# Performance work log

Hardware: AMD Instinct MI355X
Metric: run time of the kernel (lower is better)

## Reference

```python
import jax, jax.numpy as jnp
import numpy as np

F = 26          # categorical fields
VOCAB = 10000   # per-field vocab
ED = 64         # embed_dim
NUM = 13        # numerical_num
B = 4096        # batch
E = 8           # expert_num
T = 2           # task_num
D = (F + 1) * ED            # embed_output_dim = 1728
BOT = [512, 256]
TOW = [128, 64]


def setup_inputs() -> dict:
    key = jax.random.key(0)
    ks = jax.random.split(key, 20)
    s = 0.02
    inp = {}
    inp['categorical_x'] = jax.random.randint(ks[0], (B, F), 0, VOCAB, dtype=jnp.int64 if jax.config.read('jax_enable_x64') else jnp.int32)
    inp['numerical_x'] = jax.random.normal(ks[1], (B, NUM), dtype=jnp.float32)
    # shared embedding table with per-field offsets (pytorch-fm EmbeddingLayer)
    inp['offsets'] = jnp.arange(F, dtype=jnp.int32) * VOCAB
    inp['W_emb'] = jax.random.normal(ks[2], (F * VOCAB, ED), dtype=jnp.float32) * s
    # numerical linear
    inp['Wn'] = jax.random.normal(ks[3], (NUM, ED), dtype=jnp.float32) * s
    inp['bn'] = jnp.zeros((ED,), dtype=jnp.float32)
    # experts (stacked): D -> 512 -> 256, ReLU after each (BN/dropout identity at eval)
    inp['We1'] = jax.random.normal(ks[4], (E, D, BOT[0]), dtype=jnp.float32) * s
    inp['be1'] = jnp.zeros((E, BOT[0]), dtype=jnp.float32)
    inp['We2'] = jax.random.normal(ks[5], (E, BOT[0], BOT[1]), dtype=jnp.float32) * s
    inp['be2'] = jnp.zeros((E, BOT[1]), dtype=jnp.float32)
    # gates: D -> E with softmax
    inp['Wg'] = jax.random.normal(ks[6], (T, D, E), dtype=jnp.float32) * s
    inp['bg'] = jnp.zeros((T, E), dtype=jnp.float32)
    # towers: 256 -> 128 -> 64 -> 1
    inp['Wt1'] = jax.random.normal(ks[7], (T, BOT[1], TOW[0]), dtype=jnp.float32) * s
    inp['bt1'] = jnp.zeros((T, TOW[0]), dtype=jnp.float32)
    inp['Wt2'] = jax.random.normal(ks[8], (T, TOW[0], TOW[1]), dtype=jnp.float32) * s
    inp['bt2'] = jnp.zeros((T, TOW[1]), dtype=jnp.float32)
    inp['Wt3'] = jax.random.normal(ks[9], (T, TOW[1], 1), dtype=jnp.float32) * s
    inp['bt3'] = jnp.zeros((T, 1), dtype=jnp.float32)
    return inp


def reference(categorical_x, numerical_x, offsets, W_emb, Wn, bn,
              We1, be1, We2, be2, Wg, bg,
              Wt1, bt1, Wt2, bt2, Wt3, bt3):
    b = categorical_x.shape[0]
    cat_emb = W_emb[categorical_x + offsets[None, :]]          # [B, F, ED]
    num_emb = numerical_x @ Wn + bn                            # [B, ED]
    emb = jnp.concatenate([cat_emb, num_emb[:, None, :]], axis=1).reshape(b, -1)  # [B, D]
    # all experts on the shared embedding (duplicate() gives identical copies per task)
    h = jax.nn.relu(jnp.einsum('bd,edh->ebh', emb, We1) + be1[:, None, :])        # [E, B, 512]
    fea = jax.nn.relu(jnp.einsum('ebh,eho->ebo', h, We2) + be2[:, None, :])       # [E, B, 256]
    # per-task softmax gating and weighted expert mixing
    gate = jax.nn.softmax(jnp.einsum('bd,tde->tbe', emb, Wg) + bg[:, None, :], axis=-1)  # [T, B, E]
    task_fea = jnp.einsum('tbe,ebo->tbo', gate, fea)                              # [T, B, 256]
    # towers
    h1 = jax.nn.relu(jnp.einsum('tbo,toh->tbh', task_fea, Wt1) + bt1[:, None, :])
    h2 = jax.nn.relu(jnp.einsum('tbh,thk->tbk', h1, Wt2) + bt2[:, None, :])
    logits = jnp.einsum('tbk,tko->tbo', h2, Wt3) + bt3[:, None, :]                # [T, B, 1]
    return jax.nn.sigmoid(logits[..., 0])                                         # [T, B]
```

## Files before the change

kernel.cpp:

```cpp
#include <hip/hip_runtime.h>
#include <hip/hip_bf16.h>

#define B_SZ 4096
#define F_CAT 26
#define NUM_N 13
#define ED 64
#define D_DIM 1728
#define E_EXP 8
#define T_TASK 2
#define BOT0 512
#define BOT1 256
#define TOW0 128
#define TOW1 64

typedef __bf16 bf16x8 __attribute__((ext_vector_type(8)));
typedef float f32x4 __attribute__((ext_vector_type(4)));
typedef long lx2 __attribute__((ext_vector_type(2)));

__device__ __forceinline__ void gload_lds16(const void* g, void* l) {
  __builtin_amdgcn_global_load_lds(
      (const __attribute__((address_space(1))) void*)g,
      (__attribute__((address_space(3))) void*)l, 16, 0, 0);
}

#define BAR() do { asm volatile("" ::: "memory"); __builtin_amdgcn_s_barrier(); asm volatile("" ::: "memory"); } while (0)
#define VM6() asm volatile("s_waitcnt vmcnt(6)" ::: "memory")
#define VM4() asm volatile("s_waitcnt vmcnt(4)" ::: "memory")

__device__ __forceinline__ int permk(int k6) {
  return (k6 & 7) + (((k6 >> 3) & 3) << 4) + (((k6 >> 5) & 1) << 3);
}

__device__ __forceinline__ unsigned char f2e4m3(float x) {
  unsigned su = (__float_as_uint(x) >> 24) & 0x80u;
  float ax = fabsf(x);
  if (!(ax < 448.f)) return (unsigned char)(su | 0x7E);
  if (ax == 0.f) return (unsigned char)su;
  int e;
  float m = frexpf(ax, &e);
  int E = e - 1;
  if (E < -6) {
    int mi = (int)rintf(ldexpf(ax, 9));
    if (mi >= 8) return (unsigned char)(su | 0x08);
    return (unsigned char)(su | mi);
  }
  int mi = (int)rintf(ldexpf(m, 4));
  if (mi == 16) { mi = 8; E += 1; if (E > 8) return (unsigned char)(su | 0x7E); }
  return (unsigned char)(su | ((E + 7) << 3) | (mi - 8));
}

__device__ __forceinline__ void trans_tile_bf16(
    const float* __restrict__ inp, __hip_bfloat16* __restrict__ outp,
    int R, int C, int cx, int ry, float (*tile)[33])
{
  int c0 = cx * 32, r0 = ry * 32;
  int tx = threadIdx.x & 31, ty = threadIdx.x >> 5;
#pragma unroll
  for (int i = 0; i < 32; i += 8)
    tile[ty + i][tx] = inp[(size_t)(r0 + ty + i) * C + c0 + tx];
  __syncthreads();
#pragma unroll
  for (int i = 0; i < 32; i += 8)
    outp[(size_t)(c0 + ty + i) * R + r0 + tx] = __float2bfloat16(tile[tx][ty + i]);
}

__device__ __forceinline__ void trans_tile_fp8(
    const float* __restrict__ inp, unsigned char* __restrict__ outp,
    int R, int C, int cx, int ry, float (*tile)[33])
{
  int c0 = cx * 32, r0 = ry * 32;
  int tx = threadIdx.x & 31, ty = threadIdx.x >> 5;
#pragma unroll
  for (int i = 0; i < 32; i += 8)
    tile[ty + i][tx] = inp[(size_t)(r0 + ty + i) * C + c0 + tx];
  __syncthreads();
  int ki = r0 + tx;
  int outk = (ki & ~63) + permk(ki & 63);
#pragma unroll
  for (int i = 0; i < 32; i += 8)
    outp[(size_t)(c0 + ty + i) * R + outk] = f2e4m3(tile[tx][ty + i] * 16.f);
}

__global__ __launch_bounds__(256) void prep_weights(
    const float* __restrict__ We1, const float* __restrict__ We2,
    const float* __restrict__ Wg,
    unsigned char* __restrict__ We1T8, __hip_bfloat16* __restrict__ We2T,
    unsigned char* __restrict__ WgT8)
{
  __shared__ float tile[32][33];
  int id = blockIdx.x;
  if (id < 6912) {
    int z = id / 864, r = id - z * 864;
    int cx = r & 15, ry = r >> 4;
    trans_tile_fp8(We1 + (size_t)z * D_DIM * BOT0, We1T8 + (size_t)z * D_DIM * BOT0,
                   D_DIM, BOT0, cx, ry, tile);
  } else if (id < 7936) {
    int r2 = id - 6912;
    int z = r2 >> 7, r = r2 & 127;
    int cx = r & 7, ry = r >> 3;
    trans_tile_bf16(We2 + (size_t)z * BOT0 * BOT1, We2T + (size_t)z * BOT0 * BOT1,
                    BOT0, BOT1, cx, ry, tile);
  } else {
    int i = (id - 7936) * 256 + threadIdx.x;
    int n = i / D_DIM, d = i - n * D_DIM;
    int t = n >> 3, e2 = n & 7;
    int pd = (d & ~63) + permk(d & 63);
    WgT8[(size_t)n * D_DIM + pd] =
        f2e4m3(Wg[((size_t)t * D_DIM + d) * E_EXP + e2] * 16.f);
  }
}

__global__ __launch_bounds__(256) void embed_convert(
    const int* __restrict__ cat, const float* __restrict__ numx,
    const int* __restrict__ offsets, const float* __restrict__ W_emb,
    const float* __restrict__ Wn, const float* __restrict__ bnum,
    unsigned char* __restrict__ emb8)
{
  const int UNITS = 27 * 16;
  int b0 = blockIdx.x * 4;
  for (int idx = threadIdx.x; idx < 4 * UNITS; idx += 256) {
    int r = idx / UNITS, u = idx - r * UNITS;
    int f = u >> 4, d4 = (u & 15) * 4;
    int b = b0 + r;
    float4 v;
    if (f < F_CAT) {
      int row = cat[(size_t)b * F_CAT + f] + offsets[f];
      v = *reinterpret_cast<const float4*>(&W_emb[(size_t)row * ED + d4]);
    } else {
      float a0 = bnum[d4], a1 = bnum[d4 + 1], a2 = bnum[d4 + 2], a3 = bnum[d4 + 3];
#pragma unroll
      for (int n = 0; n < NUM_N; ++n) {
        float x = numx[(size_t)b * NUM_N + n];
        const float* wr = &Wn[n * ED + d4];
        a0 = fmaf(x, wr[0], a0);
        a1 = fmaf(x, wr[1], a1);
        a2 = fmaf(x, wr[2], a2);
        a3 = fmaf(x, wr[3], a3);
      }
      v = make_float4(a0, a1, a2, a3);
    }
    union { unsigned char c[4]; unsigned int w; } p8;
    p8.c[0] = f2e4m3(v.x * 16.f);
    p8.c[1] = f2e4m3(v.y * 16.f);
    p8.c[2] = f2e4m3(v.z * 16.f);
    p8.c[3] = f2e4m3(v.w * 16.f);
    int pb = (d4 & 7) + (((d4 >> 3) & 3) << 4) + (((d4 >> 5) & 1) << 3);
    *reinterpret_cast<unsigned int*>(&emb8[(size_t)b * D_DIM + f * ED + pb]) = p8.w;
  }
}

__global__ __launch_bounds__(256) void gate_mfma(
    const unsigned char* __restrict__ emb8, const unsigned char* __restrict__ WgT8,
    const float* __restrict__ bg, float* __restrict__ gate)
{
  int wid = threadIdx.x >> 6, lane = threadIdx.x & 63;
  int l15 = lane & 15, lh = lane >> 4;
  int r0 = (blockIdx.x * 4 + wid) * 16;
  f32x4 acc = {};
  const unsigned char* arow = emb8 + (size_t)(r0 + l15) * D_DIM + lh * 16;
  const unsigned char* brow = WgT8 + (size_t)l15 * D_DIM + lh * 16;
#pragma unroll 3
  for (int k = 0; k < D_DIM; k += 64) {
    lx2 av = *reinterpret_cast<const lx2*>(arow + k);
    lx2 bv = *reinterpret_cast<const lx2*>(brow + k);
    acc = __builtin_amdgcn_mfma_f32_16x16x32_fp8_fp8(av[0], bv[0], acc, 0, 0, 0);
    acc = __builtin_amdgcn_mfma_f32_16x16x32_fp8_fp8(av[1], bv[1], acc, 0, 0, 0);
  }
  int t = l15 >> 3, e = l15 & 7;
  float bv = bg[t * E_EXP + e];
#pragma unroll
  for (int r = 0; r < 4; ++r) {
    float lg = acc[r] * (1.f / 256.f) + bv;
    float m = lg;
    m = fmaxf(m, __shfl_xor(m, 1));
    m = fmaxf(m, __shfl_xor(m, 2));
    m = fmaxf(m, __shfl_xor(m, 4));
    float ex = expf(lg - m);
    float s = ex;
    s += __shfl_xor(s, 1);
    s += __shfl_xor(s, 2);
    s += __shfl_xor(s, 4);
    int row = r0 + lh * 4 + r;
    gate[((size_t)t * B_SZ + row) * E_EXP + e] = ex / s;
  }
}

__device__ __forceinline__ void mfma16(const bf16x8* a, const bf16x8* b, f32x4 (*accRows)[4]) {
#pragma unroll
  for (int i = 0; i < 4; ++i)
#pragma unroll
    for (int j = 0; j < 4; ++j)
      accRows[i][j] = __builtin_amdgcn_mfma_f32_16x16x32_bf16(a[i], b[j], accRows[i][j], 0, 0, 0);
}

__global__ __launch_bounds__(512, 2) void gemm8p_fp8(
    const unsigned char* __restrict__ A8, size_t strideAe,
    const unsigned char* __restrict__ BT8,
    const float* __restrict__ bias,
    __hip_bfloat16* __restrict__ C,
    int M, int N, int K)
{
  extern __shared__ char smem[];
  int e = blockIdx.z;
  const unsigned char* Ap = A8 + strideAe * (size_t)e;
  const unsigned char* Bp = BT8 + (size_t)e * N * K;
  const float* bp = bias + (size_t)e * N;
  __hip_bfloat16* Cp = C + (size_t)e * M * N;
  int bm0 = blockIdx.x * 256, bn0 = blockIdx.y * 256;

  int tid = threadIdx.x;
  int wid = tid >> 6, lane = tid & 63;
  int l15 = lane & 15, lh = lane >> 4;
  int wrow = (wid >> 2) * 128, wcol = (wid & 3) * 64;

  int slotc = (lh ^ (((l15 >> 3) & 1) << 1)) << 4;
  const char* rdA = smem + (wrow + l15) * 64 + slotc;
  const char* rdB = smem + 49152 + (wcol + l15) * 64 + slotc;
  char* stA = smem + (wid << 10);
  char* stB = smem + 49152 + (wid << 10);

  int srow = tid >> 2;
  int ssw = (tid & 3) ^ (((srow >> 3) & 1) << 1);
  const unsigned char* gA0 = Ap + (size_t)(bm0 + srow) * K + ssw * 16;
  const unsigned char* gA1 = Ap + (size_t)(bm0 + 128 + srow) * K + ssw * 16;
  const unsigned char* gB0 = Bp + (size_t)(bn0 + srow) * K + ssw * 16;
  const unsigned char* gB1 = Bp + (size_t)(bn0 + 128 + srow) * K + ssw * 16;

  auto STAGE = [&](int koff, int buf) {
    gload_lds16(gA0 + koff, stA + buf * 16384);
    gload_lds16(gA1 + koff, stA + buf * 16384 + 8192);
    gload_lds16(gB0 + koff, stB + buf * 16384);
    gload_lds16(gB1 + koff, stB + buf * 16384 + 8192);
  };

  f32x4 acc[8][4] = {};
  int NT = K >> 6;

  STAGE(0, 0);
  STAGE(64, 1);
  VM4();
  BAR();

  int bufc = 0, koff = 128;
  for (int T = 0; T < NT; ++T) {
    const char* As = rdA + bufc * 16384;
    const char* Bs = rdB + bufc * 16384;
    int sb = bufc >= 1 ? bufc - 1 : 2;
    lx2 va[4], vb[4];

#pragma unroll
    for (int i = 0; i < 4; ++i) va[i] = *(const lx2*)(As + i * 1024);
#pragma unroll
    for (int j = 0; j < 4; ++j) vb[j] = *(const lx2*)(Bs + j * 1024);
    STAGE(koff, sb);
    BAR();
    __builtin_amdgcn_s_setprio(1);
#pragma unroll
    for (int i = 0; i < 4; ++i)
#pragma unroll
      for (int j = 0; j < 4; ++j)
        acc[i][j] = __builtin_amdgcn_mfma_f32_16x16x32_fp8_fp8(va[i][0], vb[j][0], acc[i][j], 0, 0, 0);
#pragma unroll
    for (int i = 0; i < 4; ++i)
#pragma unroll
      for (int j = 0; j < 4; ++j)
        acc[i][j] = __builtin_amdgcn_mfma_f32_16x16x32_fp8_fp8(va[i][1], vb[j][1], acc[i][j], 0, 0, 0);
    __builtin_amdgcn_s_setprio(0);
    BAR();

#pragma unroll
    for (int i = 0; i < 4; ++i) va[i] = *(const lx2*)(As + 4096 + i * 1024);
    BAR();
    __builtin_amdgcn_s_setprio(1);
#pragma unroll
    for (int i = 0; i < 4; ++i)
#pragma unroll
      for (int j = 0; j < 4; ++j)
        acc[4 + i][j] = __builtin_amdgcn_mfma_f32_16x16x32_fp8_fp8(va[i][0], vb[j][0], acc[4 + i][j], 0, 0, 0);
#pragma unroll
    for (int i = 0; i < 4; ++i)
#pragma unroll
      for (int j = 0; j < 4; ++j)
        acc[4 + i][j] = __builtin_amdgcn_mfma_f32_16x16x32_fp8_fp8(va[i][1], vb[j][1], acc[4 + i][j], 0, 0, 0);
    __builtin_amdgcn_s_setprio(0);
    VM4();
    BAR();

    koff += 64;
    bufc = bufc == 2 ? 0 : bufc + 1;
  }

  asm volatile("s_waitcnt vmcnt(0)" ::: "memory");
  BAR();
  __hip_bfloat16* cs = (__hip_bfloat16*)smem;
#pragma unroll
  for (int nj = 0; nj < 4; ++nj) {
    int col = wcol + nj * 16 + l15;
    float bv = bp[bn0 + col];
#pragma unroll
    for (int mi = 0; mi < 8; ++mi) {
      int rb = wrow + mi * 16 + lh * 4;
#pragma unroll
      for (int r = 0; r < 4; ++r) {
        float v = acc[mi][nj][r] * (1.f / 256.f) + bv;
        cs[(size_t)(rb + r) * 256 + col] = __float2bfloat16(fmaxf(v, 0.f));
      }
    }
  }
  BAR();
  {
    int rr = tid >> 5, c8 = (tid & 31) * 8;
#pragma unroll
    for (int p = 0; p < 16; ++p) {
      int row = p * 16 + rr;
      *reinterpret_cast<uint4*>(&Cp[(size_t)(bm0 + row) * N + bn0 + c8]) =
          *reinterpret_cast<const uint4*>(&cs[(size_t)row * 256 + c8]);
    }
  }
}

__global__ __launch_bounds__(512, 2) void gemm4p(
    const __hip_bfloat16* __restrict__ A, size_t strideAe,
    const __hip_bfloat16* __restrict__ BT,
    const float* __restrict__ bias,
    __hip_bfloat16* __restrict__ C,
    int M, int N, int K)
{
  extern __shared__ char smem[];
  int e = blockIdx.z;
  const __hip_bfloat16* Ap = A + strideAe * (size_t)e;
  const __hip_bfloat16* Bp = BT + (size_t)e * N * K;
  const float* bp = bias + (size_t)e * N;
  __hip_bfloat16* Cp = C + (size_t)e * M * N;
  int bm0 = blockIdx.x * 128, bn0 = blockIdx.y * 256;

  int tid = threadIdx.x;
  int wid = tid >> 6, lane = tid & 63;
  int l15 = lane & 15, lh = lane >> 4;
  int wrow = (wid >> 2) * 64, wcol = (wid & 3) * 64;

  int slotc = (lh ^ (((l15 >> 3) & 1) << 1)) << 4;
  const char* rdA = smem + (wrow + l15) * 64 + slotc;
  const char* rdB = smem + 32768 + (wcol + l15) * 64 + slotc;
  char* stA = smem + (wid << 10);
  char* stB = smem + 32768 + (wid << 10);

  const __hip_bfloat16* gA;
  const __hip_bfloat16* gB[2];
  {
    int X = (wid << 10) + (lane << 4);
    int row = X >> 6;
    int ss = ((X >> 4) & 3) ^ (((row >> 3) & 1) << 1);
    gA = Ap + (size_t)(bm0 + row) * K + ss * 8;
#pragma unroll
    for (int j = 0; j < 2; ++j) {
      int X2 = X + (j << 13);
      int row2 = X2 >> 6;
      int ss2 = ((X2 >> 4) & 3) ^ (((row2 >> 3) & 1) << 1);
      gB[j] = Bp + (size_t)(bn0 + row2) * K + ss2 * 8;
    }
  }

  f32x4 acc[4][4] = {};
  int NT = K >> 6;

  gload_lds16(gA, stA);
#pragma unroll
  for (int j = 0; j < 2; ++j) gload_lds16(gB[j], stB + (j << 13));
  gload_lds16(gA + 32, stA + 8192);
#pragma unroll
  for (int j = 0; j < 2; ++j) gload_lds16(gB[j] + 32, stB + 16384 + (j << 13));
  gload_lds16(gA + 64, stA + 16384);
#pragma unroll
  for (int j = 0; j < 2; ++j) gload_lds16(gB[j] + 64, stB + 32768 + (j << 13));
  VM6();
  BAR();

  for (int T = 0; T < NT; ++T) {
    int pA = (T & 1) << 14, qA = pA ^ 16384;
    int pB = (T & 1) << 15, qB = pB ^ 32768;
    const char* As = rdA + pA;
    const char* Bs = rdB + pB;
    bf16x8 a[4], b[4];

#pragma unroll
    for (int i = 0; i < 4; ++i) a[i] = *(const bf16x8*)(As + i * 1024);
#pragma unroll
    for (int j = 0; j < 4; ++j) b[j] = *(const bf16x8*)(Bs + j * 1024);
    gload_lds16(gA + 96, stA + qA + 8192);
#pragma unroll
    for (int j = 0; j < 2; ++j) gload_lds16(gB[j] + 96, stB + qB + 16384 + (j << 13));
    BAR();
    __builtin_amdgcn_s_setprio(1); mfma16(a, b, acc); __builtin_amdgcn_s_setprio(0);
    VM6();
    BAR();

#pragma unroll
    for (int i = 0; i < 4; ++i) a[i] = *(const bf16x8*)(As + 8192 + i * 1024);
#pragma unroll
    for (int j = 0; j < 4; ++j) b[j] = *(const bf16x8*)(Bs + 16384 + j * 1024);
    gload_lds16(gA + 128, stA + pA);
#pragma unroll
    for (int j = 0; j < 2; ++j) gload_lds16(gB[j] + 128, stB + pB + (j << 13));
    BAR();
    __builtin_amdgcn_s_setprio(1); mfma16(a, b, acc); __builtin_amdgcn_s_setprio(0);
    VM6();
    BAR();

    gA += 64;
#pragma unroll
    for (int j = 0; j < 2; ++j) gB[j] += 64;
  }

  asm volatile("s_waitcnt vmcnt(0)" ::: "memory");
  BAR();
  __hip_bfloat16* cs = (__hip_bfloat16*)smem;
#pragma unroll
  for (int nj = 0; nj < 4; ++nj) {
    int col = wcol + nj * 16 + l15;
    float bv = bp[bn0 + col];
#pragma unroll
    for (int mi = 0; mi < 4; ++mi) {
      int rb = wrow + mi * 16 + lh * 4;
#pragma unroll
      for (int r = 0; r < 4; ++r) {
        float v = acc[mi][nj][r] + bv;
        cs[(size_t)(rb + r) * 256 + col] = __float2bfloat16(fmaxf(v, 0.f));
      }
    }
  }
  BAR();
  {
    int rr = tid >> 5, c8 = (tid & 31) * 8;
#pragma unroll
    for (int p = 0; p < 8; ++p) {
      int row = p * 16 + rr;
      *reinterpret_cast<uint4*>(&Cp[(size_t)(bm0 + row) * N + bn0 + c8]) =
          *reinterpret_cast<const uint4*>(&cs[(size_t)row * 256 + c8]);
    }
  }
}

#define TB 16
__global__ __launch_bounds__(256) void combine_tower(
    const float* __restrict__ gate, const __hip_bfloat16* __restrict__ fea,
    const float* __restrict__ Wt1, const float* __restrict__ bt1,
    const float* __restrict__ Wt2, const float* __restrict__ bt2,
    const float* __restrict__ Wt3, const float* __restrict__ bt3,
    float* __restrict__ out)
{
  int t = blockIdx.y;
  int b0 = blockIdx.x * TB;
  int tid = threadIdx.x;
  __shared__ float gs[TB][E_EXP];
  __shared__ float tf[TB][BOT1];
  __shared__ float h1[TB][TOW0];
  __shared__ float h2[TB][TOW1];
  if (tid < TB * E_EXP) {
    int bl = tid >> 3, e = tid & 7;
    gs[bl][e] = gate[((size_t)t * B_SZ + b0 + bl) * E_EXP + e];
  }
  __syncthreads();
  for (int i = tid; i < TB * BOT1; i += 256) {
    int bl = i >> 8, o = i & 255;
    float s = 0.f;
#pragma unroll
    for (int e = 0; e < E_EXP; ++e)
      s = fmaf(gs[bl][e], __bfloat162float(fea[((size_t)e * B_SZ + b0 + bl) * BOT1 + o]), s);
    tf[bl][o] = s;
  }
  __syncthreads();
  {
    int h = tid & 127, half = tid >> 7;
    float a[8] = {0, 0, 0, 0, 0, 0, 0, 0};
    for (int d = 0; d < BOT1; ++d) {
      float w = Wt1[((size_t)t * BOT1 + d) * TOW0 + h];
#pragma unroll
      for (int q = 0; q < 8; ++q) a[q] = fmaf(w, tf[half * 8 + q][d], a[q]);
    }
    float bv = bt1[t * TOW0 + h];
#pragma unroll
    for (int q = 0; q < 8; ++q) h1[half * 8 + q][h] = fmaxf(a[q] + bv, 0.f);
  }
  __syncthreads();
  {
    int h = tid & 63, qt = tid >> 6;
    float a[4] = {0, 0, 0, 0};
    for (int d = 0; d < TOW0; ++d) {
      float w = Wt2[((size_t)t * TOW0 + d) * TOW1 + h];
#pragma unroll
      for (int q = 0; q < 4; ++q) a[q] = fmaf(w, h1[qt * 4 + q][d], a[q]);
    }
    float bv = bt2[t * TOW1 + h];
#pragma unroll
    for (int q = 0; q < 4; ++q) h2[qt * 4 + q][h] = fmaxf(a[q] + bv, 0.f);
  }
  __syncthreads();
  {
    int l16 = tid & 15, bl = tid >> 4;
    float p = 0.f;
#pragma unroll
    for (int d = l16; d < TOW1; d += 16) p = fmaf(h2[bl][d], Wt3[t * TOW1 + d], p);
#pragma unroll
    for (int o = 8; o; o >>= 1) p += __shfl_down(p, o, 16);
    if (l16 == 0) {
      float lg = p + bt3[t];
      out[(size_t)t * B_SZ + b0 + bl] = 1.f / (1.f + expf(-lg));
    }
  }
}

extern "C" void kernel_launch(void* const* d_in, const int* in_sizes, int n_in,
                              void* d_out, int out_size, void* d_ws, size_t ws_size,
                              hipStream_t stream) {
  const int* cat = (const int*)d_in[0];
  const float* numx = (const float*)d_in[1];
  const int* offsets = (const int*)d_in[2];
  const float* W_emb = (const float*)d_in[3];
  const float* Wn = (const float*)d_in[4];
  const float* bnv = (const float*)d_in[5];
  const float* We1 = (const float*)d_in[6];
  const float* be1 = (const float*)d_in[7];
  const float* We2 = (const float*)d_in[8];
  const float* be2 = (const float*)d_in[9];
  const float* Wg = (const float*)d_in[10];
  const float* bg = (const float*)d_in[11];
  const float* Wt1 = (const float*)d_in[12];
  const float* bt1 = (const float*)d_in[13];
  const float* Wt2 = (const float*)d_in[14];
  const float* bt2 = (const float*)d_in[15];
  const float* Wt3 = (const float*)d_in[16];
  const float* bt3 = (const float*)d_in[17];
  float* out = (float*)d_out;

  char* ws = (char*)d_ws;
  size_t off = 0;
  auto alloc = [&](size_t bytes) {
    char* p = ws + off;
    off += (bytes + 255) & ~(size_t)255;
    return p;
  };
  unsigned char*  emb8  = (unsigned char*)alloc((size_t)B_SZ * D_DIM);
  unsigned char*  We1T8 = (unsigned char*)alloc((size_t)E_EXP * BOT0 * D_DIM);
  __hip_bfloat16* We2T  = (__hip_bfloat16*)alloc((size_t)E_EXP * BOT1 * BOT0 * 2);
  __hip_bfloat16* H     = (__hip_bfloat16*)alloc((size_t)E_EXP * B_SZ * BOT0 * 2);
  __hip_bfloat16* fea   = (__hip_bfloat16*)alloc((size_t)E_EXP * B_SZ * BOT1 * 2);
  float* gate = (float*)alloc((size_t)T_TASK * B_SZ * E_EXP * 4);
  unsigned char*  WgT8  = (unsigned char*)alloc((size_t)T_TASK * E_EXP * D_DIM);
  (void)alloc(4096);

  hipFuncSetAttribute((const void*)gemm8p_fp8,
                      hipFuncAttributeMaxDynamicSharedMemorySize, 131072);
  hipFuncSetAttribute((const void*)gemm4p,
                      hipFuncAttributeMaxDynamicSharedMemorySize, 98304);

  prep_weights<<<dim3(8044), 256, 0, stream>>>(We1, We2, Wg, We1T8, We2T, WgT8);

  embed_convert<<<dim3(B_SZ / 4), 256, 0, stream>>>(cat, numx, offsets, W_emb, Wn, bnv, emb8);

  gate_mfma<<<dim3(B_SZ / 64), 256, 0, stream>>>(emb8, WgT8, bg, gate);

  gemm8p_fp8<<<dim3(B_SZ / 256, BOT0 / 256, E_EXP), 512, 131072, stream>>>(
      emb8, (size_t)0, We1T8, be1, H, B_SZ, BOT0, D_DIM);

  gemm4p<<<dim3(B_SZ / 128, BOT1 / 256, E_EXP), 512, 98304, stream>>>(
      H, (size_t)B_SZ * BOT0, We2T, be2, fea, B_SZ, BOT1, BOT0);

  combine_tower<<<dim3(B_SZ / TB, T_TASK), 256, 0, stream>>>(
      gate, fea, Wt1, bt1, Wt2, bt2, Wt3, bt3, out);
}
```

Measured before the change: 121.7 us.

## Switch first expert GEMM to 32x32x64 scaled FP8 MFMA with matching layout

Replaces the 16x16x32 FP8 MFMA inner loop of the first expert GEMM with the gfx950 32x32x64 scaled f8f6f4 MFMA, using a unit scale. The embedding and We1 weights are rewritten into a new permuted row/K layout so that each lane's 32-byte operand comes straight from two 16-byte LDS reads. The embed kernel is reorganised so each thread writes 16 contiguous bytes, and the gate kernel's addressing is updated to the new layout. The aim is fewer MFMA instructions and LDS reads per K step, at the cost of intricate index mapping, where any mismatch would give wrong results.

```diff
diff --git a/kernel.cpp b/kernel.cpp
--- a/kernel.cpp
+++ b/kernel.cpp
@@ -15,7 +15,12 @@
 
 typedef __bf16 bf16x8 __attribute__((ext_vector_type(8)));
 typedef float f32x4 __attribute__((ext_vector_type(4)));
+typedef float f32x16 __attribute__((ext_vector_type(16)));
 typedef long lx2 __attribute__((ext_vector_type(2)));
+typedef int i32x4 __attribute__((ext_vector_type(4)));
+typedef int i32x8 __attribute__((ext_vector_type(8)));
+
+#define SCL 0x7F7F7F7F
 
 __device__ __forceinline__ void gload_lds16(const void* g, void* l) {
   __builtin_amdgcn_global_load_lds(
@@ -29,6 +34,16 @@
 
 __device__ __forceinline__ int permk(int k6) {
   return (k6 & 7) + (((k6 >> 3) & 3) << 4) + (((k6 >> 5) & 1) << 3);
+}
+
+__device__ __forceinline__ size_t mxpos(int row, int kabs, int K) {
+  int kt = kabs >> 6, kk = kabs & 63;
+  int reg = row & ~63, ro = row & 63;
+  int sub = ro >> 5, rr = ro & 31, r = rr & 15;
+  int u = ((kk >> 5) << 1) | ((rr >> 4) & 1);
+  int p = (kk >> 4) & 1;
+  int g = (sub << 1) | p;
+  return (size_t)(reg + g * 16 + r) * K + kt * 64 + u * 16 + (kk & 15);
 }
 
 __device__ __forceinline__ unsigned char f2e4m3(float x) {
@@ -64,7 +79,7 @@
     outp[(size_t)(c0 + ty + i) * R + r0 + tx] = __float2bfloat16(tile[tx][ty + i]);
 }
 
-__device__ __forceinline__ void trans_tile_fp8(
+__device__ __forceinline__ void trans_tile_fp8mx(
     const float* __restrict__ inp, unsigned char* __restrict__ outp,
     int R, int C, int cx, int ry, float (*tile)[33])
 {
@@ -75,10 +90,9 @@
     tile[ty + i][tx] = inp[(size_t)(r0 + ty + i) * C + c0 + tx];
   __syncthreads();
   int ki = r0 + tx;
-  int outk = (ki & ~63) + permk(ki & 63);
 #pragma unroll
   for (int i = 0; i < 32; i += 8)
-    outp[(size_t)(c0 + ty + i) * R + outk] = f2e4m3(tile[tx][ty + i] * 16.f);
+    outp[mxpos(c0 + ty + i, ki, R)] = f2e4m3(tile[tx][ty + i] * 16.f);
 }
 
 __global__ __launch_bounds__(256) void prep_weights(
@@ -92,8 +106,8 @@
   if (id < 6912) {
     int z = id / 864, r = id - z * 864;
     int cx = r & 15, ry = r >> 4;
-    trans_tile_fp8(We1 + (size_t)z * D_DIM * BOT0, We1T8 + (size_t)z * D_DIM * BOT0,
-                   D_DIM, BOT0, cx, ry, tile);
+    trans_tile_fp8mx(We1 + (size_t)z * D_DIM * BOT0, We1T8 + (size_t)z * D_DIM * BOT0,
+                     D_DIM, BOT0, cx, ry, tile);
   } else if (id < 7936) {
     int r2 = id - 6912;
     int z = r2 >> 7, r = r2 & 127;
@@ -116,37 +130,39 @@
     const float* __restrict__ Wn, const float* __restrict__ bnum,
     unsigned char* __restrict__ emb8)
 {
-  const int UNITS = 27 * 16;
-  int b0 = blockIdx.x * 4;
-  for (int idx = threadIdx.x; idx < 4 * UNITS; idx += 256) {
-    int r = idx / UNITS, u = idx - r * UNITS;
-    int f = u >> 4, d4 = (u & 15) * 4;
-    int b = b0 + r;
-    float4 v;
-    if (f < F_CAT) {
-      int row = cat[(size_t)b * F_CAT + f] + offsets[f];
-      v = *reinterpret_cast<const float4*>(&W_emb[(size_t)row * ED + d4]);
-    } else {
-      float a0 = bnum[d4], a1 = bnum[d4 + 1], a2 = bnum[d4 + 2], a3 = bnum[d4 + 3];
-#pragma unroll
-      for (int n = 0; n < NUM_N; ++n) {
-        float x = numx[(size_t)b * NUM_N + n];
-        const float* wr = &Wn[n * ED + d4];
-        a0 = fmaf(x, wr[0], a0);
-        a1 = fmaf(x, wr[1], a1);
-        a2 = fmaf(x, wr[2], a2);
-        a3 = fmaf(x, wr[3], a3);
-      }
-      v = make_float4(a0, a1, a2, a3);
-    }
-    union { unsigned char c[4]; unsigned int w; } p8;
-    p8.c[0] = f2e4m3(v.x * 16.f);
-    p8.c[1] = f2e4m3(v.y * 16.f);
-    p8.c[2] = f2e4m3(v.z * 16.f);
-    p8.c[3] = f2e4m3(v.w * 16.f);
-    int pb = (d4 & 7) + (((d4 >> 3) & 3) << 4) + (((d4 >> 5) & 1) << 3);
-    *reinterpret_cast<unsigned int*>(&emb8[(size_t)b * D_DIM + f * ED + pb]) = p8.w;
-  }
+  int W = blockIdx.x * 256 + threadIdx.x;
+  int prow = W / 108, ucol = W - prow * 108;
+  int f = ucol >> 2, u = ucol & 3;
+  int reg = prow & ~63, po = prow & 63;
+  int g = po >> 4, r = po & 15;
+  int sub = g >> 1, p = g & 1;
+  int h = u >> 1, rbit = u & 1;
+  int b = reg + sub * 32 + rbit * 16 + r;
+  int kk = h * 32 + p * 16;
+  float vals[16];
+  if (f < F_CAT) {
+    int row = cat[(size_t)b * F_CAT + f] + offsets[f];
+    const float4* src = reinterpret_cast<const float4*>(&W_emb[(size_t)row * ED + kk]);
+#pragma unroll
+    for (int q = 0; q < 4; ++q) {
+      float4 v = src[q];
+      vals[q * 4 + 0] = v.x; vals[q * 4 + 1] = v.y;
+      vals[q * 4 + 2] = v.z; vals[q * 4 + 3] = v.w;
+    }
+  } else {
+#pragma unroll
+    for (int j = 0; j < 16; ++j) vals[j] = bnum[kk + j];
+    for (int n = 0; n < NUM_N; ++n) {
+      float x = numx[(size_t)b * NUM_N + n];
+      const float* wr = &Wn[n * ED + kk];
+#pragma unroll
+      for (int j = 0; j < 16; ++j) vals[j] = fmaf(x, wr[j], vals[j]);
+    }
+  }
+  union { unsigned char c[16]; uint4 q; } o;
+#pragma unroll
+  for (int j = 0; j < 16; ++j) o.c[j] = f2e4m3(vals[j] * 16.f);
+  *reinterpret_cast<uint4*>(&emb8[(size_t)prow * D_DIM + f * 64 + u * 16]) = o.q;
 }
 
 __global__ __launch_bounds__(256) void gate_mfma(
@@ -157,14 +173,21 @@
   int l15 = lane & 15, lh = lane >> 4;
   int r0 = (blockIdx.x * 4 + wid) * 16;
   f32x4 acc = {};
-  const unsigned char* arow = emb8 + (size_t)(r0 + l15) * D_DIM + lh * 16;
+  int b = r0 + l15;
+  int reg = b & ~63, ro = b & 63;
+  int sub = ro >> 5, rr = ro & 31;
+  int rbit = (rr >> 4) & 1, rq = rr & 15;
+  int pgh = lh >> 1;
+  int prow = reg + (((sub << 1) | pgh) << 4) + rq;
+  const unsigned char* arow = emb8 + (size_t)prow * D_DIM + rbit * 16 + (lh & 1) * 8;
   const unsigned char* brow = WgT8 + (size_t)l15 * D_DIM + lh * 16;
 #pragma unroll 3
   for (int k = 0; k < D_DIM; k += 64) {
-    lx2 av = *reinterpret_cast<const lx2*>(arow + k);
+    long a0 = *reinterpret_cast<const long*>(arow + k);
+    long a1 = *reinterpret_cast<const long*>(arow + k + 32);
     lx2 bv = *reinterpret_cast<const lx2*>(brow + k);
-    acc = __builtin_amdgcn_mfma_f32_16x16x32_fp8_fp8(av[0], bv[0], acc, 0, 0, 0);
-    acc = __builtin_amdgcn_mfma_f32_16x16x32_fp8_fp8(av[1], bv[1], acc, 0, 0, 0);
+    acc = __builtin_amdgcn_mfma_f32_16x16x32_fp8_fp8(a0, bv[0], acc, 0, 0, 0);
+    acc = __builtin_amdgcn_mfma_f32_16x16x32_fp8_fp8(a1, bv[1], acc, 0, 0, 0);
   }
   int t = l15 >> 3, e = l15 & 7;
   float bv = bg[t * E_EXP + e];
@@ -193,7 +216,16 @@
       accRows[i][j] = __builtin_amdgcn_mfma_f32_16x16x32_bf16(a[i], b[j], accRows[i][j], 0, 0, 0);
 }
 
-__global__ __launch_bounds__(512, 2) void gemm8p_fp8(
+__device__ __forceinline__ i32x8 ld32(const char* base, int off) {
+  i32x4 a = *reinterpret_cast<const i32x4*>(base + off);
+  i32x4 b = *reinterpret_cast<const i32x4*>(base + off + 1024);
+  i32x8 r;
+  r[0] = a[0]; r[1] = a[1]; r[2] = a[2]; r[3] = a[3];
+  r[4] = b[0]; r[5] = b[1]; r[6] = b[2]; r[7] = b[3];
+  return r;
+}
+
+__global__ __launch_bounds__(512, 2) void gemm_mx(
     const unsigned char* __restrict__ A8, size_t strideAe,
     const unsigned char* __restrict__ BT8,
     const float* __restrict__ bias,
@@ -211,6 +243,7 @@
   int tid = threadIdx.x;
   int wid = tid >> 6, lane = tid & 63;
   int l15 = lane & 15, lh = lane >> 4;
+  int l31 = lane & 31, hl = lane >> 5;
   int wrow = (wid >> 2) * 128, wcol = (wid & 3) * 64;
 
   int slotc = (lh ^ (((l15 >> 3) & 1) << 1)) << 4;
@@ -233,7 +266,7 @@
     gload_lds16(gB1 + koff, stB + buf * 16384 + 8192);
   };
 
-  f32x4 acc[8][4] = {};
+  f32x16 acc[4][2] = {};
   int NT = K >> 6;
 
   STAGE(0, 0);
@@ -246,42 +279,30 @@
     const char* As = rdA + bufc * 16384;
     const char* Bs = rdB + bufc * 16384;
     int sb = bufc >= 1 ? bufc - 1 : 2;
-    lx2 va[4], vb[4];
-
-#pragma unroll
-    for (int i = 0; i < 4; ++i) va[i] = *(const lx2*)(As + i * 1024);
-#pragma unroll
-    for (int j = 0; j < 4; ++j) vb[j] = *(const lx2*)(Bs + j * 1024);
+    i32x8 va0, va1, vb0, vb1;
+
+    va0 = ld32(As, 0);
+    va1 = ld32(As, 2048);
+    vb0 = ld32(Bs, 0);
+    vb1 = ld32(Bs, 2048);
     STAGE(koff, sb);
     BAR();
     __builtin_amdgcn_s_setprio(1);
-#pragma unroll
-    for (int i = 0; i < 4; ++i)
-#pragma unroll
-      for (int j = 0; j < 4; ++j)
-        acc[i][j] = __builtin_amdgcn_mfma_f32_16x16x32_fp8_fp8(va[i][0], vb[j][0], acc[i][j], 0, 0, 0);
-#pragma unroll
-    for (int i = 0; i < 4; ++i)
-#pragma unroll
-      for (int j = 0; j < 4; ++j)
-        acc[i][j] = __builtin_amdgcn_mfma_f32_16x16x32_fp8_fp8(va[i][1], vb[j][1], acc[i][j], 0, 0, 0);
+    acc[0][0] = __builtin_amdgcn_mfma_scale_f32_32x32x64_f8f6f4(va0, vb0, acc[0][0], 0, 0, 0, SCL, 0, SCL);
+    acc[0][1] = __builtin_amdgcn_mfma_scale_f32_32x32x64_f8f6f4(va0, vb1, acc[0][1], 0, 0, 0, SCL, 0, SCL);
+    acc[1][0] = __builtin_amdgcn_mfma_scale_f32_32x32x64_f8f6f4(va1, vb0, acc[1][0], 0, 0, 0, SCL, 0, SCL);
+    acc[1][1] = __builtin_amdgcn_mfma_scale_f32_32x32x64_f8f6f4(va1, vb1, acc[1][1], 0, 0, 0, SCL, 0, SCL);
     __builtin_amdgcn_s_setprio(0);
     BAR();
 
-#pragma unroll
-    for (int i = 0; i < 4; ++i) va[i] = *(const lx2*)(As + 4096 + i * 1024);
+    va0 = ld32(As, 4096);
+    va1 = ld32(As, 4096 + 2048);
     BAR();
     __builtin_amdgcn_s_setprio(1);
-#pragma unroll
-    for (int i = 0; i < 4; ++i)
-#pragma unroll
-      for (int j = 0; j < 4; ++j)
-        acc[4 + i][j] = __builtin_amdgcn_mfma_f32_16x16x32_fp8_fp8(va[i][0], vb[j][0], acc[4 + i][j], 0, 0, 0);
-#pragma unroll
-    for (int i = 0; i < 4; ++i)
-#pragma unroll
-      for (int j = 0; j < 4; ++j)
-        acc[4 + i][j] = __builtin_amdgcn_mfma_f32_16x16x32_fp8_fp8(va[i][1], vb[j][1], acc[4 + i][j], 0, 0, 0);
+    acc[2][0] = __builtin_amdgcn_mfma_scale_f32_32x32x64_f8f6f4(va0, vb0, acc[2][0], 0, 0, 0, SCL, 0, SCL);
+    acc[2][1] = __builtin_amdgcn_mfma_scale_f32_32x32x64_f8f6f4(va0, vb1, acc[2][1], 0, 0, 0, SCL, 0, SCL);
+    acc[3][0] = __builtin_amdgcn_mfma_scale_f32_32x32x64_f8f6f4(va1, vb0, acc[3][0], 0, 0, 0, SCL, 0, SCL);
+    acc[3][1] = __builtin_amdgcn_mfma_scale_f32_32x32x64_f8f6f4(va1, vb1, acc[3][1], 0, 0, 0, SCL, 0, SCL);
     __builtin_amdgcn_s_setprio(0);
     VM4();
     BAR();
@@ -294,16 +315,17 @@
   BAR();
   __hip_bfloat16* cs = (__hip_bfloat16*)smem;
 #pragma unroll
-  for (int nj = 0; nj < 4; ++nj) {
-    int col = wcol + nj * 16 + l15;
-    float bv = bp[bn0 + col];
-#pragma unroll
-    for (int mi = 0; mi < 8; ++mi) {
-      int rb = wrow + mi * 16 + lh * 4;
-#pragma unroll
-      for (int r = 0; r < 4; ++r) {
-        float v = acc[mi][nj][r] * (1.f / 256.f) + bv;
-        cs[(size_t)(rb + r) * 256 + col] = __float2bfloat16(fmaxf(v, 0.f));
+  for (int mi = 0; mi < 4; ++mi) {
+#pragma unroll
+    for (int nj = 0; nj < 2; ++nj) {
+      int colT = wcol + nj * 32 + l31;
+      float bv = bp[bn0 + colT];
+      f32x16 a = acc[mi][nj];
+#pragma unroll
+      for (int rg = 0; rg < 16; ++rg) {
+        int rowT = wrow + mi * 32 + (rg & 3) + ((rg >> 2) << 3) + (hl << 2);
+        float v = a[rg] * (1.f / 256.f) + bv;
+        cs[(size_t)rowT * 256 + colT] = __float2bfloat16(fmaxf(v, 0.f));
       }
     }
   }
@@ -549,18 +571,19 @@
   unsigned char*  WgT8  = (unsigned char*)alloc((size_t)T_TASK * E_EXP * D_DIM);
   (void)alloc(4096);
 
-  hipFuncSetAttribute((const void*)gemm8p_fp8,
+  hipFuncSetAttribute((const void*)gemm_mx,
                       hipFuncAttributeMaxDynamicSharedMemorySize, 131072);
   hipFuncSetAttribute((const void*)gemm4p,
                       hipFuncAttributeMaxDynamicSharedMemorySize, 98304);
 
   prep_weights<<<dim3(8044), 256, 0, stream>>>(We1, We2, Wg, We1T8, We2T, WgT8);
 
-  embed_convert<<<dim3(B_SZ / 4), 256, 0, stream>>>(cat, numx, offsets, W_emb, Wn, bnv, emb8);
+  embed_convert<<<dim3(B_SZ * 108 / 256), 256, 0, stream>>>(
+      cat, numx, offsets, W_emb, Wn, bnv, emb8);
 
   gate_mfma<<<dim3(B_SZ / 64), 256, 0, stream>>>(emb8, WgT8, bg, gate);
 
-  gemm8p_fp8<<<dim3(B_SZ / 256, BOT0 / 256, E_EXP), 512, 131072, stream>>>(
+  gemm_mx<<<dim3(B_SZ / 256, BOT0 / 256, E_EXP), 512, 131072, stream>>>(
       emb8, (size_t)0, We1T8, be1, H, B_SZ, BOT0, D_DIM);
 
   gemm4p<<<dim3(B_SZ / 128, BOT1 / 256, E_EXP), 512, 98304, stream>>>(
```

After: 117.7 us. 1.03x faster.
